# Kernel tuning notes

Hardware: AMD Instinct MI355X
Metric: run time of the kernel (lower is better)

## Reference

```python
import jax, jax.numpy as jnp
import numpy as np

DIM = 256
EPS = 1e-8


def rmsnorm(y, scale):
    # full RMSNorm (p < 0): rms = ||y||_2 / sqrt(d)
    norm = jnp.linalg.norm(y, axis=-1, keepdims=True)
    rms = norm * (DIM ** -0.5)
    return scale * (y / (rms + EPS))


def setup_inputs() -> dict:
    key = jax.random.key(0)
    ks = jax.random.split(key, 12)
    d = DIM
    inp = {
        "agent": jax.random.normal(ks[0], (64, d), dtype=jnp.float32),
        "x": jax.random.normal(ks[1], (8, 8192, d), dtype=jnp.float32),
        "W_qkv": jax.random.normal(ks[2], (3 * d, d), dtype=jnp.float32) * 0.02,
        "b_qkv": jnp.zeros((3 * d,), dtype=jnp.float32),
        "W_agent": jax.random.normal(ks[3], (2 * d, d), dtype=jnp.float32) * 0.02,
        "b_agent": jnp.zeros((2 * d,), dtype=jnp.float32),
        "W_fc1": jax.random.normal(ks[4], (d, d), dtype=jnp.float32) * 0.02,
        "b_fc1": jnp.zeros((d,), dtype=jnp.float32),
        "W_fc2": jax.random.normal(ks[5], (d, d), dtype=jnp.float32) * 0.02,
        "b_fc2": jnp.zeros((d,), dtype=jnp.float32),
        "norm_scale": jnp.ones((d,), dtype=jnp.float32),
    }
    return inp


def reference(agent, x, W_qkv, b_qkv, W_agent, b_agent, W_fc1, b_fc1, W_fc2, b_fc2, norm_scale):
    sc = DIM ** -0.5
    # qkv projection of x: [B, N, 3d] -> q, k, v each [B, N, d]
    qkv = x @ W_qkv.T + b_qkv
    q, k, v = jnp.split(qkv, 3, axis=-1)
    # agent projection: [K, 2d] -> q_agent, k_agent each [K, d]
    qa_ka = agent @ W_agent.T + b_agent
    q_agent, k_agent = jnp.split(qa_ka, 2, axis=-1)
    # stage 1: agents attend over tokens  -> [B, K, N]
    attn1 = jax.nn.softmax(jnp.einsum('kd,bnd->bkn', q_agent, k) * sc, axis=-1)
    v1 = jnp.einsum('bkn,bnd->bkd', attn1, v)  # [B, K, d]
    v1 = v1 @ W_fc1.T + b_fc1
    # stage 2: tokens attend over agents -> [B, N, K]
    attn2 = jax.nn.softmax(jnp.einsum('bnd,kd->bnk', q, k_agent) * sc, axis=-1)
    v2 = jnp.einsum('bnk,bkd->bnd', attn2, v1)  # [B, N, d]
    v2 = v2 @ W_fc2.T + b_fc2
    return rmsnorm(v2 + x, norm_scale)
```

## Files before the change

kernel.cpp:

```cpp
#include <hip/hip_runtime.h>
#include <hip/hip_bf16.h>

typedef __attribute__((ext_vector_type(4))) float f32x4;
typedef __attribute__((ext_vector_type(8))) short s16x8;
typedef __attribute__((ext_vector_type(4))) short s16x4;

__device__ __forceinline__ unsigned short f2bf(float f) {
    unsigned int u; __builtin_memcpy(&u, &f, 4);
    u += 0x7fffu + ((u >> 16) & 1u);
    return (unsigned short)(u >> 16);
}
__device__ __forceinline__ float bf2f(unsigned short h) {
    unsigned int u = ((unsigned int)h) << 16;
    float f; __builtin_memcpy(&f, &u, 4);
    return f;
}
__device__ __forceinline__ s16x8 pack8(f32x4 a, f32x4 b) {
    s16x8 r;
    r[0] = (short)f2bf(a[0]); r[1] = (short)f2bf(a[1]);
    r[2] = (short)f2bf(a[2]); r[3] = (short)f2bf(a[3]);
    r[4] = (short)f2bf(b[0]); r[5] = (short)f2bf(b[1]);
    r[6] = (short)f2bf(b[2]); r[7] = (short)f2bf(b[3]);
    return r;
}

__global__ __launch_bounds__(256) void build_M2(
    const float* __restrict__ W_qkv, const float* __restrict__ b_qkv,
    const float* __restrict__ agent, const float* __restrict__ W_agent,
    const float* __restrict__ b_agent,
    const float* __restrict__ W_fc1, const float* __restrict__ W_fc2,
    unsigned short* __restrict__ MS, float* __restrict__ cbias,
    unsigned short* __restrict__ Wb)
{
    const int i = blockIdx.x;
    const int t = threadIdx.x;
    if (i >= 128) {
        const int R0 = (i - 128) * 4;
        #pragma unroll
        for (int rr = 0; rr < 4; ++rr) {
            const int R = R0 + rr;
            const float* src = (R < 256) ? W_qkv + (size_t)(512 + R) * 256
                             : (R < 512) ? W_fc1 + (size_t)(R - 256) * 256
                                         : W_fc2 + (size_t)(R - 512) * 256;
            Wb[(size_t)R * 256 + t] = f2bf(src[t]);
        }
        return;
    }
    __shared__ float ag[256];
    __shared__ float qs[256];
    const int a = i & 63;
    const bool isS1 = (i < 64);
    ag[t] = agent[(size_t)a * 256 + t];
    __syncthreads();
    const int tp = isS1 ? t : 256 + t;
    {
        const float* wr = W_agent + (size_t)tp * 256;
        float q = 0.f;
        #pragma unroll 4
        for (int d = 0; d < 256; d += 4) {
            f32x4 wv = *(const f32x4*)(wr + d);
            q += ag[d] * wv[0] + ag[d + 1] * wv[1] + ag[d + 2] * wv[2] + ag[d + 3] * wv[3];
        }
        qs[t] = (q + b_agent[tp]) * 0.0625f;
    }
    __syncthreads();
    const float* W  = W_qkv + (isS1 ? 256 * 256 : 0);
    const float* bb = b_qkv + (isS1 ? 256 : 0);
    float acc = 0.f, cb = 0.f;
    for (int dout = 0; dout < 256; ++dout) {
        const float q = qs[dout];
        acc += q * W[(size_t)dout * 256 + t];
        cb  += q * bb[dout];
    }
    MS[i * 256 + t] = f2bf(acc);
    if (t == 0) cbias[i] = cb;
}

__global__ __launch_bounds__(256) void xproj2(
    const float* __restrict__ x,
    const unsigned short* __restrict__ MS,
    const float* __restrict__ cbias,
    float* __restrict__ S1T,
    unsigned short* __restrict__ P2,
    float* __restrict__ mpart, float* __restrict__ lpart)
{
    __shared__ alignas(16) unsigned short As[64 * 256];
    const int tid = threadIdx.x, lane = tid & 63, w = tid >> 6;
    const int lr = lane & 15, lq = lane >> 4;
    const long m0 = (long)blockIdx.x * 64;

    {
        const int k0 = (tid & 31) * 8;
        #pragma unroll
        for (int j = 0; j < 8; ++j) {
            const int row = (tid >> 5) + j * 8;
            const float* s = x + (m0 + row) * 256 + k0;
            f32x4 f0 = *(const f32x4*)s;
            f32x4 f1 = *(const f32x4*)(s + 4);
            *(s16x8*)((char*)As + row * 512 + ((k0 * 2) ^ ((row & 7) << 4))) = pack8(f0, f1);
        }
    }
    __syncthreads();

    f32x4 acc[4][2];
    const f32x4 zero = {0.f, 0.f, 0.f, 0.f};
    #pragma unroll
    for (int rf = 0; rf < 4; ++rf)
        #pragma unroll
        for (int j = 0; j < 2; ++j)
            acc[rf][j] = zero;

    #pragma unroll
    for (int ks = 0; ks < 8; ++ks) {
        const int kb = ks * 64 + lq * 16;
        s16x8 areg[4];
        #pragma unroll
        for (int rf = 0; rf < 4; ++rf) {
            const int row = rf * 16 + lr;
            areg[rf] = *(const s16x8*)((const char*)As + row * 512 + (kb ^ ((row & 7) << 4)));
        }
        s16x8 bfr[2];
        #pragma unroll
        for (int j = 0; j < 2; ++j) {
            const int msrow = j * 64 + w * 16 + lr;
            bfr[j] = *(const s16x8*)((const char*)MS + (size_t)msrow * 512 + kb);
        }
        #pragma unroll
        for (int rf = 0; rf < 4; ++rf)
            #pragma unroll
            for (int j = 0; j < 2; ++j)
                acc[rf][j] = __builtin_amdgcn_mfma_f32_16x16x32_bf16(
                    areg[rf], bfr[j], acc[rf][j], 0, 0, 0);
    }

    {
        const int a = w * 16 + lr;
        const float bv = cbias[a];
        float mx = -1e30f;
        #pragma unroll
        for (int rf = 0; rf < 4; ++rf)
            #pragma unroll
            for (int r = 0; r < 4; ++r) {
                const float v = acc[rf][0][r] + bv;
                S1T[(m0 + rf * 16 + lq * 4 + r) * 64 + a] = v;
                mx = fmaxf(mx, v);
            }
        mx = fmaxf(mx, __shfl_xor(mx, 16));
        mx = fmaxf(mx, __shfl_xor(mx, 32));
        float sm = 0.f;
        #pragma unroll
        for (int rf = 0; rf < 4; ++rf)
            #pragma unroll
            for (int r = 0; r < 4; ++r)
                sm += __expf(acc[rf][0][r] + bv - mx);
        sm += __shfl_xor(sm, 16);
        sm += __shfl_xor(sm, 32);
        if (lq == 0) {
            mpart[(size_t)blockIdx.x * 64 + a] = mx;
            lpart[(size_t)blockIdx.x * 64 + a] = sm;
        }
    }

    __syncthreads();
    {
        float* SC = (float*)As;
        const int a = w * 16 + lr;
        const float bv = cbias[64 + a];
        #pragma unroll
        for (int rf = 0; rf < 4; ++rf)
            #pragma unroll
            for (int r = 0; r < 4; ++r) {
                const int n = rf * 16 + lq * 4 + r;
                SC[n * 68 + a] = acc[rf][1][r] + bv;
            }
    }
    __syncthreads();
    {
        const float* SC = (const float*)As;
        const int t4 = lane >> 2, q = lane & 3;
        const int nl = w * 16 + t4;
        f32x4 sv[4];
        #pragma unroll
        for (int j = 0; j < 4; ++j) sv[j] = *(const f32x4*)&SC[nl * 68 + q * 16 + j * 4];
        float mx = -1e30f;
        #pragma unroll
        for (int j = 0; j < 4; ++j)
            #pragma unroll
            for (int e = 0; e < 4; ++e) mx = fmaxf(mx, sv[j][e]);
        mx = fmaxf(mx, __shfl_xor(mx, 1));
        mx = fmaxf(mx, __shfl_xor(mx, 2));
        float p[16];
        float sm = 0.f;
        #pragma unroll
        for (int j = 0; j < 4; ++j)
            #pragma unroll
            for (int e = 0; e < 4; ++e) {
                p[j * 4 + e] = __expf(sv[j][e] - mx);
                sm += p[j * 4 + e];
            }
        sm += __shfl_xor(sm, 1);
        sm += __shfl_xor(sm, 2);
        const float rs = 1.f / sm;
        s16x8 o0, o1;
        #pragma unroll
        for (int e = 0; e < 8; ++e) o0[e] = (short)f2bf(p[e] * rs);
        #pragma unroll
        for (int e = 0; e < 8; ++e) o1[e] = (short)f2bf(p[8 + e] * rs);
        const int swz = (nl & 7) << 4;
        char* row = (char*)P2 + (m0 + nl) * 128;
        *(s16x8*)(row + ((q * 32) ^ swz)) = o0;
        *(s16x8*)(row + ((q * 32 + 16) ^ swz)) = o1;
    }
}

__global__ __launch_bounds__(256) void pv_mfma2(
    const float* __restrict__ S1T,
    const float* __restrict__ x,
    const float* __restrict__ mpart,
    const float* __restrict__ lpart,
    float* __restrict__ y_part)
{
    __shared__ alignas(16) unsigned short P_lds[64 * 128];
    __shared__ alignas(16) unsigned short XT[128 * 136];
    const int tid = threadIdx.x, lane = tid & 63, w = tid >> 6;
    const int lr = lane & 15, lq = lane >> 4;
    const int c = blockIdx.x, dh = blockIdx.y, b = blockIdx.z;
    const int a4 = (tid & 15) * 4;

    f32x4 m4, l4;
    {
        float* scratch = (float*)XT;
        const int a = tid & 63, s4 = tid >> 6;
        const size_t bb = (size_t)b * 128;
        float M = -1e30f;
        for (int cc = s4; cc < 128; cc += 4)
            M = fmaxf(M, mpart[(bb + cc) * 64 + a]);
        float L = 0.f;
        for (int cc = s4; cc < 128; cc += 4) {
            const size_t idx = (bb + cc) * 64 + a;
            L += lpart[idx] * __expf(mpart[idx] - M);
        }
        scratch[tid] = M;
        scratch[256 + tid] = L;
        __syncthreads();
        if (tid < 64) {
            float Mm = scratch[tid];
            #pragma unroll
            for (int ss = 1; ss < 4; ++ss) Mm = fmaxf(Mm, scratch[ss * 64 + tid]);
            float Ll = 0.f;
            #pragma unroll
            for (int ss = 0; ss < 4; ++ss)
                Ll += scratch[256 + ss * 64 + tid] * __expf(scratch[ss * 64 + tid] - Mm);
            scratch[512 + tid] = Mm;
            scratch[576 + tid] = 1.0f / Ll;
        }
        __syncthreads();
        #pragma unroll
        for (int j = 0; j < 4; ++j) {
            m4[j] = scratch[512 + a4 + j];
            l4[j] = scratch[576 + a4 + j];
        }
        __syncthreads();
    }

    f32x4 acc[4][2];
    const f32x4 zero = {0.f, 0.f, 0.f, 0.f};
    #pragma unroll
    for (int rf = 0; rf < 4; ++rf)
        #pragma unroll
        for (int cf = 0; cf < 2; ++cf)
            acc[rf][cf] = zero;

    for (int kt = 0; kt < 4; ++kt) {
        const size_t ng0 = (size_t)b * 8192 + c * 512 + kt * 128;
        #pragma unroll
        for (int pass = 0; pass < 4; ++pass) {
            const int np = 2 * (tid >> 4) + pass * 32;
            const float* s = S1T + (ng0 + np) * 64 + a4;
            f32x4 s0 = *(const f32x4*)s;
            f32x4 s1 = *(const f32x4*)(s + 64);
            #pragma unroll
            for (int j = 0; j < 4; ++j) {
                const int a = a4 + j;
                const float p0 = __expf(s0[j] - m4[j]) * l4[j];
                const float p1 = __expf(s1[j] - m4[j]) * l4[j];
                const unsigned int pk = (unsigned int)f2bf(p0) | ((unsigned int)f2bf(p1) << 16);
                *(unsigned int*)((char*)P_lds + a * 256 + ((np * 2) ^ (((a >> 1) & 7) << 4))) = pk;
            }
        }
        {
            const int nh = tid >> 2;
            const int dq = tid & 3;
            const float* xbase = x + (ng0 + 2 * nh) * 256 + dh * 128;
            #pragma unroll
            for (int pass = 0; pass < 8; ++pass) {
                const int dl0 = pass * 16 + dq * 4;
                f32x4 xa = *(const f32x4*)(xbase + dl0);
                f32x4 xb = *(const f32x4*)(xbase + 256 + dl0);
                #pragma unroll
                for (int jj = 0; jj < 4; ++jj) {
                    const unsigned int pk = (unsigned int)f2bf(xa[jj]) | ((unsigned int)f2bf(xb[jj]) << 16);
                    *(unsigned int*)((char*)XT + (dl0 + jj) * 272 + nh * 4) = pk;
                }
            }
        }
        __syncthreads();
        #pragma unroll
        for (int ks = 0; ks < 4; ++ks) {
            const int kbn = ks * 64 + lq * 16;
            s16x8 af[4], bfv[2];
            #pragma unroll
            for (int rf = 0; rf < 4; ++rf) {
                const int row = rf * 16 + lr;
                af[rf] = *(const s16x8*)((const char*)P_lds + row * 256 + (kbn ^ (((row >> 1) & 7) << 4)));
            }
            #pragma unroll
            for (int cf = 0; cf < 2; ++cf) {
                const int dl = w * 32 + cf * 16 + lr;
                bfv[cf] = *(const s16x8*)((const char*)XT + dl * 272 + kbn);
            }
            #pragma unroll
            for (int rf = 0; rf < 4; ++rf)
                #pragma unroll
                for (int cf = 0; cf < 2; ++cf)
                    acc[rf][cf] = __builtin_amdgcn_mfma_f32_16x16x32_bf16(
                        af[rf], bfv[cf], acc[rf][cf], 0, 0, 0);
        }
        __syncthreads();
    }
    #pragma unroll
    for (int rf = 0; rf < 4; ++rf)
        #pragma unroll
        for (int cf = 0; cf < 2; ++cf)
            #pragma unroll
            for (int r = 0; r < 4; ++r) {
                const int a = rf * 16 + lq * 4 + r;
                const int d = dh * 128 + w * 32 + cf * 16 + lr;
                y_part[(((size_t)b * 16 + c) * 64 + a) * 256 + d] = acc[rf][cf][r];
            }
}

__global__ __launch_bounds__(256) void chain_fused(
    const float* __restrict__ y_part,
    const unsigned short* __restrict__ Wb,
    const float* __restrict__ b_qkv,
    const float* __restrict__ b_fc1,
    const float* __restrict__ b_fc2,
    float* __restrict__ uu)
{
    __shared__ alignas(16) unsigned short A0[64 * 256];
    __shared__ alignas(16) unsigned short A1[64 * 256];
    const int tid = threadIdx.x, lane = tid & 63, w = tid >> 6;
    const int lr = lane & 15, lq = lane >> 4;
    const int b = blockIdx.x;

    {
        const float* yp = y_part + (size_t)b * 16 * 64 * 256;
        f32x4 r16[16];
        const f32x4 zero = {0.f, 0.f, 0.f, 0.f};
        #pragma unroll
        for (int j = 0; j < 16; ++j) r16[j] = zero;
        for (int c = 0; c < 16; ++c) {
            const float* base = yp + (size_t)c * 16384 + tid * 4;
            #pragma unroll
            for (int j = 0; j < 16; ++j)
                r16[j] += *(const f32x4*)(base + j * 1024);
        }
        #pragma unroll
        for (int j = 0; j < 16; ++j) {
            const int a = j * 4 + (tid >> 6);
            const int d0 = (tid & 63) * 4;
            s16x4 pk;
            #pragma unroll
            for (int e = 0; e < 4; ++e) pk[e] = (short)f2bf(r16[j][e]);
            *(s16x4*)((char*)A0 + a * 512 + ((d0 * 2) ^ ((a & 7) << 4))) = pk;
        }
    }
    __syncthreads();

    unsigned short* bufA = A0;
    unsigned short* bufB = A1;
    for (int s = 0; s < 3; ++s) {
        const unsigned short* W = Wb + (size_t)s * 65536;
        const float* bias = (s == 0) ? (b_qkv + 512) : (s == 1) ? b_fc1 : b_fc2;
        f32x4 acc[4][4];
        const f32x4 zero = {0.f, 0.f, 0.f, 0.f};
        #pragma unroll
        for (int rf = 0; rf < 4; ++rf)
            #pragma unroll
            for (int cf = 0; cf < 4; ++cf)
                acc[rf][cf] = zero;
        #pragma unroll
        for (int ks = 0; ks < 8; ++ks) {
            const int kb = ks * 64 + lq * 16;
            s16x8 af[4], bf[4];
            #pragma unroll
            for (int rf = 0; rf < 4; ++rf) {
                const int row = rf * 16 + lr;
                af[rf] = *(const s16x8*)((const char*)bufA + row * 512 + (kb ^ ((row & 7) << 4)));
            }
            #pragma unroll
            for (int cf = 0; cf < 4; ++cf) {
                const int col = w * 64 + cf * 16 + lr;
                bf[cf] = *(const s16x8*)((const char*)W + (size_t)col * 512 + kb);
            }
            #pragma unroll
            for (int rf = 0; rf < 4; ++rf)
                #pragma unroll
                for (int cf = 0; cf < 4; ++cf)
                    acc[rf][cf] = __builtin_amdgcn_mfma_f32_16x16x32_bf16(
                        af[rf], bf[cf], acc[rf][cf], 0, 0, 0);
        }
        if (s < 2) {
            #pragma unroll
            for (int cf = 0; cf < 4; ++cf) {
                const int col = w * 64 + cf * 16 + lr;
                const float bv = bias[col];
                #pragma unroll
                for (int rf = 0; rf < 4; ++rf)
                    #pragma unroll
                    for (int r = 0; r < 4; ++r) {
                        const int a = rf * 16 + lq * 4 + r;
                        *(unsigned short*)((char*)bufB + a * 512 + ((col * 2) ^ ((a & 7) << 4)))
                            = f2bf(acc[rf][cf][r] + bv);
                    }
            }
            __syncthreads();
            unsigned short* t = bufA; bufA = bufB; bufB = t;
        } else {
            #pragma unroll
            for (int cf = 0; cf < 4; ++cf) {
                const int col = w * 64 + cf * 16 + lr;
                const float bv = bias[col];
                #pragma unroll
                for (int rf = 0; rf < 4; ++rf)
                    #pragma unroll
                    for (int r = 0; r < 4; ++r) {
                        const int a = rf * 16 + lq * 4 + r;
                        uu[((size_t)b * 64 + a) * 256 + col] = acc[rf][cf][r] + bv;
                    }
            }
        }
    }
}

__global__ __launch_bounds__(256) void stage2_final(const unsigned short* __restrict__ P2,
                                                    const float* __restrict__ uu,
                                                    const float* __restrict__ x,
                                                    const float* __restrict__ nscale,
                                                    float* __restrict__ out)
{
    __shared__ alignas(16) unsigned short uT[256 * 64];
    __shared__ alignas(16) unsigned short P[64 * 64];
    __shared__ float ssq[4][64];
    const int tid = threadIdx.x, lane = tid & 63, w = tid >> 6;
    const int lr = lane & 15, lq = lane >> 4;
    const int b = blockIdx.x >> 7;
    const long n0 = (long)blockIdx.x * 64;

    {
        const int pr = tid >> 3;
        const int sub = tid & 7;
        const float* u0 = uu + ((size_t)b * 64 + 2 * pr) * 256;
        #pragma unroll
        for (int pass = 0; pass < 8; ++pass) {
            const int d0 = pass * 32 + sub * 4;
            f32x4 ua = *(const f32x4*)(u0 + d0);
            f32x4 ub = *(const f32x4*)(u0 + 256 + d0);
            #pragma unroll
            for (int jj = 0; jj < 4; ++jj) {
                const int d = d0 + jj;
                const unsigned int pk = (unsigned int)f2bf(ua[jj]) | ((unsigned int)f2bf(ub[jj]) << 16);
                *(unsigned int*)((char*)uT + d * 128 + ((pr * 4) ^ ((d & 7) << 4))) = pk;
            }
        }
    }
    {
        const int row = tid & 63, seg = tid >> 6;
        const char* src = (const char*)P2 + (n0 + row) * 128 + seg * 32;
        s16x8 v0 = *(const s16x8*)src;
        s16x8 v1 = *(const s16x8*)(src + 16);
        *(s16x8*)((char*)P + row * 128 + seg * 32) = v0;
        *(s16x8*)((char*)P + row * 128 + seg * 32 + 16) = v1;
    }
    __syncthreads();

    f32x4 acc[4][4];
    const f32x4 zero = {0.f, 0.f, 0.f, 0.f};
    #pragma unroll
    for (int rf = 0; rf < 4; ++rf)
        #pragma unroll
        for (int cf = 0; cf < 4; ++cf)
            acc[rf][cf] = zero;
    #pragma unroll
    for (int ks = 0; ks < 2; ++ks) {
        const int kb = ks * 64 + lq * 16;
        s16x8 af[4], bfv[4];
        #pragma unroll
        for (int rf = 0; rf < 4; ++rf) {
            const int dR = w * 64 + rf * 16 + lr;
            af[rf] = *(const s16x8*)((const char*)uT + dR * 128 + (kb ^ ((dR & 7) << 4)));
        }
        #pragma unroll
        for (int cf = 0; cf < 4; ++cf) {
            const int nR = cf * 16 + lr;
            bfv[cf] = *(const s16x8*)((const char*)P + nR * 128 + (kb ^ ((nR & 7) << 4)));
        }
        #pragma unroll
        for (int rf = 0; rf < 4; ++rf)
            #pragma unroll
            for (int cf = 0; cf < 4; ++cf)
                acc[rf][cf] = __builtin_amdgcn_mfma_f32_16x16x32_bf16(
                    af[rf], bfv[cf], acc[rf][cf], 0, 0, 0);
    }

    float part[4] = {0.f, 0.f, 0.f, 0.f};
    #pragma unroll
    for (int cf = 0; cf < 4; ++cf) {
        const long n = n0 + cf * 16 + lr;
        #pragma unroll
        for (int rf = 0; rf < 4; ++rf) {
            const int d0 = w * 64 + rf * 16 + lq * 4;
            const f32x4 xr = *(const f32x4*)&x[n * 256 + d0];
            acc[rf][cf] += xr;
            part[cf] += acc[rf][cf][0] * acc[rf][cf][0] + acc[rf][cf][1] * acc[rf][cf][1]
                      + acc[rf][cf][2] * acc[rf][cf][2] + acc[rf][cf][3] * acc[rf][cf][3];
        }
    }
    #pragma unroll
    for (int cf = 0; cf < 4; ++cf) {
        float s = part[cf];
        s += __shfl_xor(s, 16);
        s += __shfl_xor(s, 32);
        if (lq == 0) ssq[w][cf * 16 + lr] = s;
    }
    __syncthreads();

    #pragma unroll
    for (int cf = 0; cf < 4; ++cf) {
        const int tokl = cf * 16 + lr;
        const float tot = ssq[0][tokl] + ssq[1][tokl] + ssq[2][tokl] + ssq[3][tokl];
        const float inv = 1.f / (sqrtf(tot) * 0.0625f + 1e-8f);
        const long n = n0 + tokl;
        #pragma unroll
        for (int rf = 0; rf < 4; ++rf) {
            const int d0 = w * 64 + rf * 16 + lq * 4;
            const f32x4 sc4 = *(const f32x4*)&nscale[d0];
            f32x4 o = sc4 * acc[rf][cf] * inv;
            *(f32x4*)&out[n * 256 + d0] = o;
        }
    }
}

extern "C" void kernel_launch(void* const* d_in, const int* in_sizes, int n_in,
                              void* d_out, int out_size, void* d_ws, size_t ws_size,
                              hipStream_t stream)
{
    const float* agent   = (const float*)d_in[0];
    const float* x       = (const float*)d_in[1];
    const float* W_qkv   = (const float*)d_in[2];
    const float* b_qkv   = (const float*)d_in[3];
    const float* W_agent = (const float*)d_in[4];
    const float* b_agent = (const float*)d_in[5];
    const float* W_fc1   = (const float*)d_in[6];
    const float* b_fc1   = (const float*)d_in[7];
    const float* W_fc2   = (const float*)d_in[8];
    const float* b_fc2   = (const float*)d_in[9];
    const float* nscale  = (const float*)d_in[10];
    float* out = (float*)d_out;

    char* wsp = (char*)d_ws;
    size_t off = 0;
    auto alloc = [&](size_t n) { void* p = wsp + off; off += (n + 255) & ~(size_t)255; return p; };

    unsigned short* MS = (unsigned short*)alloc(128UL * 256 * 2);
    float*  cbias  = (float*)alloc(128UL * 4);
    unsigned short* Wb = (unsigned short*)alloc(3UL * 256 * 256 * 2);
    float*  S1T    = (float*)alloc(65536UL * 64 * 4);
    unsigned short* P2 = (unsigned short*)alloc(65536UL * 64 * 2);
    float*  mpart  = (float*)alloc(1024UL * 64 * 4);
    float*  lpart  = (float*)alloc(1024UL * 64 * 4);
    float*  y_part = (float*)alloc(8UL * 16 * 64 * 256 * 4);
    float*  uu     = (float*)alloc(512UL * 256 * 4);

    build_M2<<<320, 256, 0, stream>>>(W_qkv, b_qkv, agent, W_agent, b_agent,
                                      W_fc1, W_fc2, MS, cbias, Wb);
    xproj2<<<1024, 256, 0, stream>>>(x, MS, cbias, S1T, P2, mpart, lpart);
    pv_mfma2<<<dim3(16, 2, 8), 256, 0, stream>>>(S1T, x, mpart, lpart, y_part);
    chain_fused<<<8, 256, 0, stream>>>(y_part, Wb, b_qkv, b_fc1, b_fc2, uu);
    stage2_final<<<1024, 256, 0, stream>>>(P2, uu, x, nscale, out);
}
```

Baseline: 138.9 us.

## Split token chunks and agent rows across more blocks in pv and chain kernels

pv_mfma2 now processes 256 tokens per block instead of 512, doubling its grid to 512 blocks and producing 32 partial sums per batch. chain_fused is split over agent-row groups of 16 (grid 4x8 instead of 8), so each block reduces only its rows and runs a smaller MFMA chain. Both changes aim to fill more compute units on small, latency-bound kernels. In exchange, the partial-sum buffer doubles, each chain block reads more partials, and each chain block reloads the full weight matrices.

```diff
diff --git a/kernel.cpp b/kernel.cpp
--- a/kernel.cpp
+++ b/kernel.cpp
@@ -271,8 +271,8 @@
         for (int cf = 0; cf < 2; ++cf)
             acc[rf][cf] = zero;
 
-    for (int kt = 0; kt < 4; ++kt) {
-        const size_t ng0 = (size_t)b * 8192 + c * 512 + kt * 128;
+    for (int kt = 0; kt < 2; ++kt) {
+        const size_t ng0 = (size_t)b * 8192 + c * 256 + kt * 128;
         #pragma unroll
         for (int pass = 0; pass < 4; ++pass) {
             const int np = 2 * (tid >> 4) + pass * 32;
@@ -336,7 +336,7 @@
             for (int r = 0; r < 4; ++r) {
                 const int a = rf * 16 + lq * 4 + r;
                 const int d = dh * 128 + w * 32 + cf * 16 + lr;
-                y_part[(((size_t)b * 16 + c) * 64 + a) * 256 + d] = acc[rf][cf][r];
+                y_part[(((size_t)b * 32 + c) * 64 + a) * 256 + d] = acc[rf][cf][r];
             }
 }
 
@@ -348,31 +348,31 @@
     const float* __restrict__ b_fc2,
     float* __restrict__ uu)
 {
-    __shared__ alignas(16) unsigned short A0[64 * 256];
-    __shared__ alignas(16) unsigned short A1[64 * 256];
+    __shared__ alignas(16) unsigned short A0[16 * 256];
+    __shared__ alignas(16) unsigned short A1[16 * 256];
     const int tid = threadIdx.x, lane = tid & 63, w = tid >> 6;
     const int lr = lane & 15, lq = lane >> 4;
-    const int b = blockIdx.x;
-
-    {
-        const float* yp = y_part + (size_t)b * 16 * 64 * 256;
-        f32x4 r16[16];
+    const int rg = blockIdx.x, b = blockIdx.y;
+    const int a0 = rg * 16;
+
+    {
+        const int d0 = lane * 4;
+        f32x4 r4[4];
         const f32x4 zero = {0.f, 0.f, 0.f, 0.f};
         #pragma unroll
-        for (int j = 0; j < 16; ++j) r16[j] = zero;
-        for (int c = 0; c < 16; ++c) {
-            const float* base = yp + (size_t)c * 16384 + tid * 4;
-            #pragma unroll
-            for (int j = 0; j < 16; ++j)
-                r16[j] += *(const f32x4*)(base + j * 1024);
-        }
-        #pragma unroll
-        for (int j = 0; j < 16; ++j) {
-            const int a = j * 4 + (tid >> 6);
-            const int d0 = (tid & 63) * 4;
+        for (int j = 0; j < 4; ++j) r4[j] = zero;
+        for (int c = 0; c < 32; ++c) {
+            const float* base = y_part + (((size_t)b * 32 + c) * 64 + a0 + w * 4) * 256 + d0;
+            #pragma unroll
+            for (int j = 0; j < 4; ++j)
+                r4[j] += *(const f32x4*)(base + (size_t)j * 256);
+        }
+        #pragma unroll
+        for (int j = 0; j < 4; ++j) {
+            const int a = w * 4 + j;
             s16x4 pk;
             #pragma unroll
-            for (int e = 0; e < 4; ++e) pk[e] = (short)f2bf(r16[j][e]);
+            for (int e = 0; e < 4; ++e) pk[e] = (short)f2bf(r4[j][e]);
             *(s16x4*)((char*)A0 + a * 512 + ((d0 * 2) ^ ((a & 7) << 4))) = pk;
         }
     }
@@ -383,33 +383,24 @@
     for (int s = 0; s < 3; ++s) {
         const unsigned short* W = Wb + (size_t)s * 65536;
         const float* bias = (s == 0) ? (b_qkv + 512) : (s == 1) ? b_fc1 : b_fc2;
-        f32x4 acc[4][4];
+        f32x4 acc[4];
         const f32x4 zero = {0.f, 0.f, 0.f, 0.f};
         #pragma unroll
-        for (int rf = 0; rf < 4; ++rf)
-            #pragma unroll
-            for (int cf = 0; cf < 4; ++cf)
-                acc[rf][cf] = zero;
+        for (int cf = 0; cf < 4; ++cf) acc[cf] = zero;
         #pragma unroll
         for (int ks = 0; ks < 8; ++ks) {
             const int kb = ks * 64 + lq * 16;
-            s16x8 af[4], bf[4];
-            #pragma unroll
-            for (int rf = 0; rf < 4; ++rf) {
-                const int row = rf * 16 + lr;
-                af[rf] = *(const s16x8*)((const char*)bufA + row * 512 + (kb ^ ((row & 7) << 4)));
-            }
+            const int row = lr;
+            s16x8 af = *(const s16x8*)((const char*)bufA + row * 512 + (kb ^ ((row & 7) << 4)));
+            s16x8 bf[4];
             #pragma unroll
             for (int cf = 0; cf < 4; ++cf) {
                 const int col = w * 64 + cf * 16 + lr;
                 bf[cf] = *(const s16x8*)((const char*)W + (size_t)col * 512 + kb);
             }
             #pragma unroll
-            for (int rf = 0; rf < 4; ++rf)
-                #pragma unroll
-                for (int cf = 0; cf < 4; ++cf)
-                    acc[rf][cf] = __builtin_amdgcn_mfma_f32_16x16x32_bf16(
-                        af[rf], bf[cf], acc[rf][cf], 0, 0, 0);
+            for (int cf = 0; cf < 4; ++cf)
+                acc[cf] = __builtin_amdgcn_mfma_f32_16x16x32_bf16(af, bf[cf], acc[cf], 0, 0, 0);
         }
         if (s < 2) {
             #pragma unroll
@@ -417,13 +408,11 @@
                 const int col = w * 64 + cf * 16 + lr;
                 const float bv = bias[col];
                 #pragma unroll
-                for (int rf = 0; rf < 4; ++rf)
-                    #pragma unroll
-                    for (int r = 0; r < 4; ++r) {
-                        const int a = rf * 16 + lq * 4 + r;
-                        *(unsigned short*)((char*)bufB + a * 512 + ((col * 2) ^ ((a & 7) << 4)))
-                            = f2bf(acc[rf][cf][r] + bv);
-                    }
+                for (int r = 0; r < 4; ++r) {
+                    const int a = lq * 4 + r;
+                    *(unsigned short*)((char*)bufB + a * 512 + ((col * 2) ^ ((a & 7) << 4)))
+                        = f2bf(acc[cf][r] + bv);
+                }
             }
             __syncthreads();
             unsigned short* t = bufA; bufA = bufB; bufB = t;
@@ -433,12 +422,10 @@
                 const int col = w * 64 + cf * 16 + lr;
                 const float bv = bias[col];
                 #pragma unroll
-                for (int rf = 0; rf < 4; ++rf)
-                    #pragma unroll
-                    for (int r = 0; r < 4; ++r) {
-                        const int a = rf * 16 + lq * 4 + r;
-                        uu[((size_t)b * 64 + a) * 256 + col] = acc[rf][cf][r] + bv;
-                    }
+                for (int r = 0; r < 4; ++r) {
+                    const int a = a0 + lq * 4 + r;
+                    uu[((size_t)b * 64 + a) * 256 + col] = acc[cf][r] + bv;
+                }
             }
         }
     }
@@ -580,13 +567,13 @@
     unsigned short* P2 = (unsigned short*)alloc(65536UL * 64 * 2);
     float*  mpart  = (float*)alloc(1024UL * 64 * 4);
     float*  lpart  = (float*)alloc(1024UL * 64 * 4);
-    float*  y_part = (float*)alloc(8UL * 16 * 64 * 256 * 4);
+    float*  y_part = (float*)alloc(8UL * 32 * 64 * 256 * 4);
     float*  uu     = (float*)alloc(512UL * 256 * 4);
 
     build_M2<<<320, 256, 0, stream>>>(W_qkv, b_qkv, agent, W_agent, b_agent,
                                       W_fc1, W_fc2, MS, cbias, Wb);
     xproj2<<<1024, 256, 0, stream>>>(x, MS, cbias, S1T, P2, mpart, lpart);
-    pv_mfma2<<<dim3(16, 2, 8), 256, 0, stream>>>(S1T, x, mpart, lpart, y_part);
-    chain_fused<<<8, 256, 0, stream>>>(y_part, Wb, b_qkv, b_fc1, b_fc2, uu);
+    pv_mfma2<<<dim3(32, 2, 8), 256, 0, stream>>>(S1T, x, mpart, lpart, y_part);
+    chain_fused<<<dim3(4, 8), 256, 0, stream>>>(y_part, Wb, b_qkv, b_fc1, b_fc2, uu);
     stage2_final<<<1024, 256, 0, stream>>>(P2, uu, x, nscale, out);
 }
```

Measured after the change: 121.1 us, median of 2. 12.8% less time.
